# Kernel tuning notes

Hardware: AMD Instinct MI355X
Metric: run time of the kernel (lower is better)

## Reference

```python
import jax, jax.numpy as jnp
import numpy as np

B, BEV = 2, 128
Q = BEV * BEV          # 16384 BEV queries
C, H, L, P = 256, 8, 1, 4
D = C // H             # 32 per-head dim


def setup_inputs() -> dict:
    key = jax.random.key(0)
    ks = jax.random.split(key, 14)
    s = 0.02
    return {
        "query": jax.random.normal(ks[0], (B, Q, C), jnp.float32),
        "value": jax.random.normal(ks[1], (B, Q, C), jnp.float32),
        "identity": jax.random.normal(ks[2], (B, Q, C), jnp.float32),
        "query_pos": jax.random.normal(ks[3], (B, Q, C), jnp.float32),
        "reference_points": jax.random.uniform(ks[4], (B, Q, L, 2), jnp.float32),
        "spatial_shapes": jnp.array([[BEV, BEV]], jnp.int32),
        "level_start_index": jnp.array([0], jnp.int32),
        "Wv": jax.random.normal(ks[5], (C, C), jnp.float32) * s,
        "bv": jnp.zeros((C,), jnp.float32),
        "Woff": jax.random.normal(ks[6], (C, H * L * P * 2), jnp.float32) * s,
        "boff": jax.random.normal(ks[7], (H * L * P * 2,), jnp.float32) * s,
        "Ww": jax.random.normal(ks[8], (C, H * L * P), jnp.float32) * s,
        "bw": jnp.zeros((H * L * P,), jnp.float32),
        "Wo": jax.random.normal(ks[9], (C, C), jnp.float32) * s,
        "bo": jnp.zeros((C,), jnp.float32),
    }


def _deform_attn(q, v, reference_points, shapes_np, Wv, bv, Woff, boff, Ww, bw, Wo, bo):
    b, nq, _ = q.shape
    v = v @ Wv + bv                                             # value_proj
    off = (q @ Woff + boff).reshape(b, nq, H, L, P, 2)          # sampling offsets
    attn = jax.nn.softmax((q @ Ww + bw).reshape(b, nq, H, L * P), axis=-1)
    attn = attn.reshape(b, nq, H, L, P)
    # offset normalizer is (W, H) per level
    norm = jnp.asarray(shapes_np[:, ::-1], jnp.float32)         # [L, 2]
    loc = reference_points[:, :, None, :, None, :] + off / norm[None, None, None, :, None, :]

    out = jnp.zeros((b, H, nq, D), jnp.float32)
    start = 0
    for l in range(L):
        Hl, Wl = int(shapes_np[l, 0]), int(shapes_np[l, 1])
        N = Hl * Wl
        vl = v[:, start:start + N].reshape(b, N, H, D).transpose(0, 2, 1, 3)  # [b,H,N,D]
        start += N
        ll = loc[:, :, :, l]                                    # [b,nq,H,P,2] in [0,1]
        # grid_sample(align_corners=False): pixel coord = loc*size - 0.5
        x = ll[..., 0] * Wl - 0.5
        y = ll[..., 1] * Hl - 0.5
        x0 = jnp.floor(x); y0 = jnp.floor(y)
        dx = x - x0; dy = y - y0
        x0i = x0.astype(jnp.int32); y0i = y0.astype(jnp.int32)

        def gather(ix, iy):
            valid = (ix >= 0) & (ix < Wl) & (iy >= 0) & (iy < Hl)  # zero padding
            idx = jnp.clip(iy, 0, Hl - 1) * Wl + jnp.clip(ix, 0, Wl - 1)
            idx = idx.transpose(0, 2, 1, 3).reshape(b, H, nq * P)
            g = jnp.take_along_axis(vl, idx[..., None], axis=2)   # [b,H,nq*P,D]
            return g * valid.transpose(0, 2, 1, 3).reshape(b, H, nq * P, 1)

        def cw(w):  # corner weight -> [b,H,nq*P,1]
            return w.transpose(0, 2, 1, 3).reshape(b, H, nq * P, 1)

        samp = (gather(x0i, y0i) * cw((1 - dx) * (1 - dy))
                + gather(x0i + 1, y0i) * cw(dx * (1 - dy))
                + gather(x0i, y0i + 1) * cw((1 - dx) * dy)
                + gather(x0i + 1, y0i + 1) * cw(dx * dy))
        samp = samp.reshape(b, H, nq, P, D)
        aw = attn[:, :, :, l].transpose(0, 2, 1, 3)             # [b,H,nq,P]
        out = out + jnp.einsum('bhqpd,bhqp->bhqd', samp, aw)

    out = out.transpose(0, 2, 1, 3).reshape(b, nq, C)
    return out @ Wo + bo                                        # output_proj


def reference(query, value, identity, query_pos, reference_points, spatial_shapes,
              level_start_index, Wv, bv, Woff, boff, Ww, bw, Wo, bo):
    shapes_np = np.asarray(spatial_shapes)                      # static level shapes
    q = query + query_pos
    out = _deform_attn(q, value, reference_points, shapes_np,
                       Wv, bv, Woff, boff, Ww, bw, Wo, bo)
    return out + identity
```

## Files before the change

### kernel.cpp

```cpp
#include <hip/hip_runtime.h>
#include <hip/hip_bf16.h>
#include <stdint.h>

#define Q_TOT 32768
#define CC 256
#define GRID_W 128
#define GRID_H 128

typedef __attribute__((ext_vector_type(8))) short short8;
typedef __attribute__((ext_vector_type(4))) float floatx4;

__device__ __forceinline__ ushort f2bf(float f) {
    union { float f; uint32_t u; } v; v.f = f;
    uint32_t r = (v.u + 0x7fffu + ((v.u >> 16) & 1u)) >> 16;
    return (ushort)r;
}
__device__ __forceinline__ float bf2f(ushort s) {
    union { uint32_t u; float f; } v; v.u = ((uint32_t)s) << 16;
    return v.f;
}
__device__ __forceinline__ void bf2x2(uint32_t u, float& lo, float& hi) {
    union { uint32_t u; float f; } a, b;
    a.u = u << 16; b.u = u & 0xffff0000u;
    lo = a.f; hi = b.f;
}
__device__ __forceinline__ void async_load16(const void* g, void* l) {
    __builtin_amdgcn_global_load_lds(
        reinterpret_cast<const __attribute__((address_space(1))) uint32_t*>(
            reinterpret_cast<uintptr_t>(g)),
        reinterpret_cast<__attribute__((address_space(3))) uint32_t*>(
            reinterpret_cast<uintptr_t>(l)),
        16, 0, 0);
}

__global__ __launch_bounds__(256)
void prep_convert(const float* __restrict__ q, const float* __restrict__ qp,
                  const float* __restrict__ val,
                  ushort* __restrict__ qsum, ushort* __restrict__ vbf)
{
    const int total = (Q_TOT * CC) / 4;
    for (int idx = blockIdx.x * blockDim.x + threadIdx.x; idx < 2 * total;
         idx += gridDim.x * blockDim.x) {
        if (idx < total) {
            float4 a = ((const float4*)q)[idx];
            float4 b = ((const float4*)qp)[idx];
            ushort4 o;
            o.x = f2bf(a.x + b.x); o.y = f2bf(a.y + b.y);
            o.z = f2bf(a.z + b.z); o.w = f2bf(a.w + b.w);
            ((ushort4*)qsum)[idx] = o;
        } else {
            int j = idx - total;
            float4 a = ((const float4*)val)[j];
            ushort4 o;
            o.x = f2bf(a.x); o.y = f2bf(a.y); o.z = f2bf(a.z); o.w = f2bf(a.w);
            ((ushort4*)vbf)[j] = o;
        }
    }
}

__global__ __launch_bounds__(256)
void prep_weights(const float* __restrict__ Wv, const float* __restrict__ Wo,
                  const float* __restrict__ Woff, const float* __restrict__ Ww,
                  const float* __restrict__ boff, const float* __restrict__ bw,
                  ushort* __restrict__ WvT, ushort* __restrict__ WoT,
                  ushort* __restrict__ WowT, float* __restrict__ bias_ow)
{
    int idx = blockIdx.x * blockDim.x + threadIdx.x;
    if (idx < 65536) {
        int n = idx >> 8, k = idx & 255;
        WvT[idx] = f2bf(Wv[k * 256 + n]);
    } else if (idx < 131072) {
        int t = idx - 65536; int n = t >> 8, k = t & 255;
        WoT[t] = f2bf(Wo[k * 256 + n]);
    } else if (idx < 155648) {
        int t = idx - 131072; int n = t >> 8, k = t & 255;
        float v = (n < 64) ? Woff[k * 64 + n] : Ww[k * 32 + (n - 64)];
        WowT[t] = f2bf(v);
    } else if (idx < 155744) {
        int t = idx - 155648;
        bias_ow[t] = (t < 64) ? boff[t] : bw[t - 64];
    }
}

template <int BM, int BN, int WAVE_M, int WAVE_N, bool OUT_BF16>
__global__ __launch_bounds__(WAVE_M * WAVE_N * 64, 2)
void gemm_bf16(const ushort* __restrict__ A, const ushort* __restrict__ Bt,
               const float* __restrict__ bias, const float* __restrict__ res,
               void* __restrict__ Cout, int M, int N)
{
    constexpr int K = 256;
    constexpr int NC = K / 32;
    constexpr int NW = WAVE_M * WAVE_N;
    constexpr int GA = BM / 16;
    constexpr int GB = BN / 16;
    constexpr int TM = BM / WAVE_M / 16;
    constexpr int TN = BN / WAVE_N / 16;
    __shared__ ushort As[BM * K];
    __shared__ ushort Bs[BN * K];

    const int tid = threadIdx.x;
    const int lane = tid & 63;
    const int wave = tid >> 6;
    const int wm = wave / WAVE_N;
    const int wn = wave % WAVE_N;
    const int quad = lane >> 4;
    const int m16 = lane & 15;
    const int lrow = lane >> 2;
    const int lkk = (lane & 3) * 8;

    const int row0 = blockIdx.y * BM;
    const int col0 = blockIdx.x * BN;

    #pragma unroll
    for (int t = 0; t < (NC * GA) / NW; ++t) {
        const int idx = t * NW + wave;
        const int c = idx / GA, g = idx % GA;
        const ushort* src = A + (size_t)(row0 + g * 16 + lrow) * K + c * 32 + lkk;
        async_load16(src, &As[(c * GA + g) * 512]);
    }
    #pragma unroll
    for (int t = 0; t < (NC * GB) / NW; ++t) {
        const int idx = t * NW + wave;
        const int c = idx / GB, g = idx % GB;
        const ushort* src = Bt + (size_t)(col0 + g * 16 + lrow) * K + c * 32 + lkk;
        async_load16(src, &Bs[(c * GB + g) * 512]);
    }
    __syncthreads();

    floatx4 acc[TM][TN] = {};
    #pragma unroll
    for (int c = 0; c < NC; ++c) {
        short8 af[TM], bf[TN];
        #pragma unroll
        for (int i = 0; i < TM; ++i)
            af[i] = *(const short8*)&As[((c * GA + wm * TM + i) * 16 + m16) * 32 + quad * 8];
        #pragma unroll
        for (int j = 0; j < TN; ++j)
            bf[j] = *(const short8*)&Bs[((c * GB + wn * TN + j) * 16 + m16) * 32 + quad * 8];
        #pragma unroll
        for (int i = 0; i < TM; ++i)
            #pragma unroll
            for (int j = 0; j < TN; ++j)
                acc[i][j] = __builtin_amdgcn_mfma_f32_16x16x32_bf16(
                    af[i], bf[j], acc[i][j], 0, 0, 0);
    }

    #pragma unroll
    for (int i = 0; i < TM; ++i) {
        #pragma unroll
        for (int j = 0; j < TN; ++j) {
            const int gcol = col0 + (wn * TN + j) * 16 + m16;
            const float bb = bias[gcol];
            #pragma unroll
            for (int r = 0; r < 4; ++r) {
                const int grow = row0 + (wm * TM + i) * 16 + quad * 4 + r;
                float v = acc[i][j][r] + bb;
                if (res) v += res[(size_t)grow * N + gcol];
                if constexpr (OUT_BF16)
                    ((ushort*)Cout)[(size_t)grow * N + gcol] = f2bf(v);
                else
                    ((float*)Cout)[(size_t)grow * N + gcol] = v;
            }
        }
    }
}

#define QB 8
__global__ __launch_bounds__(256)
void sample_kernel(const ushort* __restrict__ v2,
                   const ushort* __restrict__ ow,
                   const float* __restrict__ ref,
                   ushort* __restrict__ out)
{
    const int tid = threadIdx.x;
    const int ql = tid >> 5;
    const int h  = (tid >> 2) & 7;
    const int dg = tid & 3;
    const int q = blockIdx.x * QB + ql;
    const int b = q >> 14;

    const ushort* op = ow + (size_t)q * 96 + h * 8;
    const uint4 oraw = *(const uint4*)op;
    float offs[8];
    bf2x2(oraw.x, offs[0], offs[1]);
    bf2x2(oraw.y, offs[2], offs[3]);
    bf2x2(oraw.z, offs[4], offs[5]);
    bf2x2(oraw.w, offs[6], offs[7]);

    const uint2 wraw = *(const uint2*)(ow + (size_t)q * 96 + 64 + h * 4);
    float w0, w1, w2, w3;
    bf2x2(wraw.x, w0, w1);
    bf2x2(wraw.y, w2, w3);
    float m = fmaxf(fmaxf(w0, w1), fmaxf(w2, w3));
    float e0 = __expf(w0 - m), e1 = __expf(w1 - m), e2 = __expf(w2 - m), e3 = __expf(w3 - m);
    float inv = 1.f / (e0 + e1 + e2 + e3);
    float aw[4] = {e0 * inv, e1 * inv, e2 * inv, e3 * inv};

    const float rx = ref[(size_t)q * 2 + 0];
    const float ry = ref[(size_t)q * 2 + 1];
    const ushort* vb = v2 + (size_t)b * 16384 * 256 + h * 32 + dg * 8;

    float acc[8] = {};
    #pragma unroll
    for (int p = 0; p < 4; ++p) {
        float x = rx * (float)GRID_W + offs[p * 2 + 0] - 0.5f;
        float y = ry * (float)GRID_H + offs[p * 2 + 1] - 0.5f;
        float x0f = floorf(x), y0f = floorf(y);
        float dx = x - x0f, dy = y - y0f;
        int x0 = (int)x0f, y0 = (int)y0f;
        int x1 = x0 + 1, y1 = y0 + 1;
        float vx0 = (x0 >= 0 && x0 < GRID_W) ? 1.f : 0.f;
        float vx1 = (x1 >= 0 && x1 < GRID_W) ? 1.f : 0.f;
        float vy0 = (y0 >= 0 && y0 < GRID_H) ? 1.f : 0.f;
        float vy1 = (y1 >= 0 && y1 < GRID_H) ? 1.f : 0.f;
        int xc0 = min(max(x0, 0), GRID_W - 1), xc1 = min(max(x1, 0), GRID_W - 1);
        int yc0 = min(max(y0, 0), GRID_H - 1), yc1 = min(max(y1, 0), GRID_H - 1);
        float cw00 = aw[p] * (1.f - dx) * (1.f - dy) * vx0 * vy0;
        float cw10 = aw[p] * dx * (1.f - dy) * vx1 * vy0;
        float cw01 = aw[p] * (1.f - dx) * dy * vx0 * vy1;
        float cw11 = aw[p] * dx * dy * vx1 * vy1;
        const int base0 = yc0 * GRID_W, base1 = yc1 * GRID_W;
        const uint4 r00 = *(const uint4*)(vb + (size_t)(base0 + xc0) * 256);
        const uint4 r10 = *(const uint4*)(vb + (size_t)(base0 + xc1) * 256);
        const uint4 r01 = *(const uint4*)(vb + (size_t)(base1 + xc0) * 256);
        const uint4 r11 = *(const uint4*)(vb + (size_t)(base1 + xc1) * 256);
        float lo, hi;
        bf2x2(r00.x, lo, hi); acc[0] += cw00 * lo; acc[1] += cw00 * hi;
        bf2x2(r00.y, lo, hi); acc[2] += cw00 * lo; acc[3] += cw00 * hi;
        bf2x2(r00.z, lo, hi); acc[4] += cw00 * lo; acc[5] += cw00 * hi;
        bf2x2(r00.w, lo, hi); acc[6] += cw00 * lo; acc[7] += cw00 * hi;
        bf2x2(r10.x, lo, hi); acc[0] += cw10 * lo; acc[1] += cw10 * hi;
        bf2x2(r10.y, lo, hi); acc[2] += cw10 * lo; acc[3] += cw10 * hi;
        bf2x2(r10.z, lo, hi); acc[4] += cw10 * lo; acc[5] += cw10 * hi;
        bf2x2(r10.w, lo, hi); acc[6] += cw10 * lo; acc[7] += cw10 * hi;
        bf2x2(r01.x, lo, hi); acc[0] += cw01 * lo; acc[1] += cw01 * hi;
        bf2x2(r01.y, lo, hi); acc[2] += cw01 * lo; acc[3] += cw01 * hi;
        bf2x2(r01.z, lo, hi); acc[4] += cw01 * lo; acc[5] += cw01 * hi;
        bf2x2(r01.w, lo, hi); acc[6] += cw01 * lo; acc[7] += cw01 * hi;
        bf2x2(r11.x, lo, hi); acc[0] += cw11 * lo; acc[1] += cw11 * hi;
        bf2x2(r11.y, lo, hi); acc[2] += cw11 * lo; acc[3] += cw11 * hi;
        bf2x2(r11.z, lo, hi); acc[4] += cw11 * lo; acc[5] += cw11 * hi;
        bf2x2(r11.w, lo, hi); acc[6] += cw11 * lo; acc[7] += cw11 * hi;
    }

    uint4 o;
    o.x = ((uint32_t)f2bf(acc[1]) << 16) | f2bf(acc[0]);
    o.y = ((uint32_t)f2bf(acc[3]) << 16) | f2bf(acc[2]);
    o.z = ((uint32_t)f2bf(acc[5]) << 16) | f2bf(acc[4]);
    o.w = ((uint32_t)f2bf(acc[7]) << 16) | f2bf(acc[6]);
    *(uint4*)(out + (size_t)q * 256 + h * 32 + dg * 8) = o;
}

extern "C" void kernel_launch(void* const* d_in, const int* in_sizes, int n_in,
                              void* d_out, int out_size, void* d_ws, size_t ws_size,
                              hipStream_t stream) {
    const float* query     = (const float*)d_in[0];
    const float* value     = (const float*)d_in[1];
    const float* identity  = (const float*)d_in[2];
    const float* query_pos = (const float*)d_in[3];
    const float* refpts    = (const float*)d_in[4];
    const float* Wv   = (const float*)d_in[7];
    const float* bv   = (const float*)d_in[8];
    const float* Woff = (const float*)d_in[9];
    const float* boff = (const float*)d_in[10];
    const float* Ww   = (const float*)d_in[11];
    const float* bw   = (const float*)d_in[12];
    const float* Wo   = (const float*)d_in[13];
    const float* bo   = (const float*)d_in[14];
    float* out = (float*)d_out;

    char* ws = (char*)d_ws;
    ushort* qsum_bf  = (ushort*)(ws);
    ushort* value_bf = (ushort*)(ws + 16777216);
    ushort* v2_bf    = (ushort*)(ws + 33554432);
    ushort* ow_bf    = (ushort*)(ws + 50331648);
    ushort* samp_bf  = (ushort*)(ws + 56623104);
    ushort* WvT      = (ushort*)(ws + 73400320);
    ushort* WoT      = (ushort*)(ws + 73531392);
    ushort* WowT     = (ushort*)(ws + 73662464);
    float*  bias_ow  = (float*)(ws + 73711616);

    prep_convert<<<8192, 256, 0, stream>>>(query, query_pos, value, qsum_bf, value_bf);
    prep_weights<<<609, 256, 0, stream>>>(Wv, Wo, Woff, Ww, boff, bw,
                                          WvT, WoT, WowT, bias_ow);
    gemm_bf16<64, 64, 2, 2, true><<<dim3(4, 512), 256, 0, stream>>>(
        value_bf, WvT, bv, nullptr, v2_bf, Q_TOT, 256);
    gemm_bf16<64, 96, 2, 2, true><<<dim3(1, 512), 256, 0, stream>>>(
        qsum_bf, WowT, bias_ow, nullptr, ow_bf, Q_TOT, 96);
    sample_kernel<<<dim3(Q_TOT / QB), 256, 0, stream>>>(v2_bf, ow_bf, refpts, samp_bf);
    gemm_bf16<64, 64, 2, 2, false><<<dim3(4, 512), 256, 0, stream>>>(
        samp_bf, WoT, bo, identity, out, Q_TOT, 256);
}
```

Baseline: 271.5 us.

## Replace LDS-staged GEMM with single-wave register-direct MFMA GEMM

The GEMM kernel no longer stages A and B tiles through LDS with async global-to-LDS loads and a barrier. Each 64-thread block now loads its MFMA fragments straight from global memory into registers and computes a 64x64 (or 64x48) tile. The aim is to drop LDS traffic, the barrier and the LDS occupancy limit. The cost is that operands are no longer shared across waves in a block, so global and L2 reads rise, and the per-lane 16-byte loads are strided by the row length.

Result: slower. 289.8 us (+6.7%).

```diff
diff --git a/kernel.cpp b/kernel.cpp
--- a/kernel.cpp
+++ b/kernel.cpp
@@ -23,14 +23,6 @@
     union { uint32_t u; float f; } a, b;
     a.u = u << 16; b.u = u & 0xffff0000u;
     lo = a.f; hi = b.f;
-}
-__device__ __forceinline__ void async_load16(const void* g, void* l) {
-    __builtin_amdgcn_global_load_lds(
-        reinterpret_cast<const __attribute__((address_space(1))) uint32_t*>(
-            reinterpret_cast<uintptr_t>(g)),
-        reinterpret_cast<__attribute__((address_space(3))) uint32_t*>(
-            reinterpret_cast<uintptr_t>(l)),
-        16, 0, 0);
 }
 
 __global__ __launch_bounds__(256)
@@ -82,61 +74,32 @@
     }
 }
 
-template <int BM, int BN, int WAVE_M, int WAVE_N, bool OUT_BF16>
-__global__ __launch_bounds__(WAVE_M * WAVE_N * 64, 2)
-void gemm_bf16(const ushort* __restrict__ A, const ushort* __restrict__ Bt,
-               const float* __restrict__ bias, const float* __restrict__ res,
-               void* __restrict__ Cout, int M, int N)
+template <int TM, int TN, bool OUT_BF16>
+__global__ __launch_bounds__(64)
+void gemm_reg(const ushort* __restrict__ A, const ushort* __restrict__ Bt,
+              const float* __restrict__ bias, const float* __restrict__ res,
+              void* __restrict__ Cout, int M, int N)
 {
     constexpr int K = 256;
-    constexpr int NC = K / 32;
-    constexpr int NW = WAVE_M * WAVE_N;
-    constexpr int GA = BM / 16;
-    constexpr int GB = BN / 16;
-    constexpr int TM = BM / WAVE_M / 16;
-    constexpr int TN = BN / WAVE_N / 16;
-    __shared__ ushort As[BM * K];
-    __shared__ ushort Bs[BN * K];
-
-    const int tid = threadIdx.x;
-    const int lane = tid & 63;
-    const int wave = tid >> 6;
-    const int wm = wave / WAVE_N;
-    const int wn = wave % WAVE_N;
+    const int lane = threadIdx.x;
     const int quad = lane >> 4;
     const int m16 = lane & 15;
-    const int lrow = lane >> 2;
-    const int lkk = (lane & 3) * 8;
-
-    const int row0 = blockIdx.y * BM;
-    const int col0 = blockIdx.x * BN;
-
-    #pragma unroll
-    for (int t = 0; t < (NC * GA) / NW; ++t) {
-        const int idx = t * NW + wave;
-        const int c = idx / GA, g = idx % GA;
-        const ushort* src = A + (size_t)(row0 + g * 16 + lrow) * K + c * 32 + lkk;
-        async_load16(src, &As[(c * GA + g) * 512]);
-    }
-    #pragma unroll
-    for (int t = 0; t < (NC * GB) / NW; ++t) {
-        const int idx = t * NW + wave;
-        const int c = idx / GB, g = idx % GB;
-        const ushort* src = Bt + (size_t)(col0 + g * 16 + lrow) * K + c * 32 + lkk;
-        async_load16(src, &Bs[(c * GB + g) * 512]);
-    }
-    __syncthreads();
+    const int row0 = blockIdx.y * (TM * 16);
+    const int col0 = blockIdx.x * (TN * 16);
+
+    const ushort* Ap = A + (size_t)(row0 + m16) * K + quad * 8;
+    const ushort* Bp = Bt + (size_t)(col0 + m16) * K + quad * 8;
 
     floatx4 acc[TM][TN] = {};
     #pragma unroll
-    for (int c = 0; c < NC; ++c) {
+    for (int c = 0; c < K / 32; ++c) {
         short8 af[TM], bf[TN];
         #pragma unroll
         for (int i = 0; i < TM; ++i)
-            af[i] = *(const short8*)&As[((c * GA + wm * TM + i) * 16 + m16) * 32 + quad * 8];
+            af[i] = *(const short8*)(Ap + (size_t)i * 16 * K + c * 32);
         #pragma unroll
         for (int j = 0; j < TN; ++j)
-            bf[j] = *(const short8*)&Bs[((c * GB + wn * TN + j) * 16 + m16) * 32 + quad * 8];
+            bf[j] = *(const short8*)(Bp + (size_t)j * 16 * K + c * 32);
         #pragma unroll
         for (int i = 0; i < TM; ++i)
             #pragma unroll
@@ -149,11 +112,11 @@
     for (int i = 0; i < TM; ++i) {
         #pragma unroll
         for (int j = 0; j < TN; ++j) {
-            const int gcol = col0 + (wn * TN + j) * 16 + m16;
+            const int gcol = col0 + j * 16 + m16;
             const float bb = bias[gcol];
             #pragma unroll
             for (int r = 0; r < 4; ++r) {
-                const int grow = row0 + (wm * TM + i) * 16 + quad * 4 + r;
+                const int grow = row0 + i * 16 + quad * 4 + r;
                 float v = acc[i][j][r] + bb;
                 if (res) v += res[(size_t)grow * N + gcol];
                 if constexpr (OUT_BF16)
@@ -283,11 +246,11 @@
     prep_convert<<<8192, 256, 0, stream>>>(query, query_pos, value, qsum_bf, value_bf);
     prep_weights<<<609, 256, 0, stream>>>(Wv, Wo, Woff, Ww, boff, bw,
                                           WvT, WoT, WowT, bias_ow);
-    gemm_bf16<64, 64, 2, 2, true><<<dim3(4, 512), 256, 0, stream>>>(
+    gemm_reg<4, 4, true><<<dim3(4, 512), 64, 0, stream>>>(
         value_bf, WvT, bv, nullptr, v2_bf, Q_TOT, 256);
-    gemm_bf16<64, 96, 2, 2, true><<<dim3(1, 512), 256, 0, stream>>>(
+    gemm_reg<4, 3, true><<<dim3(2, 512), 64, 0, stream>>>(
         qsum_bf, WowT, bias_ow, nullptr, ow_bf, Q_TOT, 96);
     sample_kernel<<<dim3(Q_TOT / QB), 256, 0, stream>>>(v2_bf, ow_bf, refpts, samp_bf);
-    gemm_bf16<64, 64, 2, 2, false><<<dim3(4, 512), 256, 0, stream>>>(
+    gemm_reg<4, 4, false><<<dim3(4, 512), 64, 0, stream>>>(
         samp_bf, WoT, bo, identity, out, Q_TOT, 256);
 }
```
